# Optimization experiments

Measured on AMD Instinct MI355X. Metric: run time of the kernel, lower is better.

Reference implementation:

```python
import jax, jax.numpy as jnp
import numpy as np

N_NODES = 100000
N_EDGES = 3200000
IN_DIM = 256
HIDDEN = 128
OUT_DIM = 64


def setup_inputs() -> dict:
    key = jax.random.key(0)
    k = jax.random.split(key, 6)
    x = jax.random.normal(k[0], (N_NODES, IN_DIM), dtype=jnp.float32)
    adj_vals = jax.random.uniform(k[1], (N_EDGES,), dtype=jnp.float32)
    # glorot init as in the original
    s1 = np.sqrt(6.0 / (IN_DIM + HIDDEN)).astype(np.float32)
    s2 = np.sqrt(6.0 / (HIDDEN + OUT_DIM)).astype(np.float32)
    w1 = jax.random.uniform(k[2], (IN_DIM, HIDDEN), dtype=jnp.float32, minval=-s1, maxval=s1)
    w2 = jax.random.uniform(k[3], (HIDDEN, OUT_DIM), dtype=jnp.float32, minval=-s2, maxval=s2)
    edge_src = jax.random.randint(k[4], (N_EDGES,), 0, N_NODES, dtype=jnp.int32)
    edge_dst = jax.random.randint(k[5], (N_EDGES,), 0, N_NODES, dtype=jnp.int32)
    return {"x": x, "adj_vals": adj_vals, "w1": w1, "w2": w2,
            "edge_src": edge_src, "edge_dst": edge_dst}


def _spmm(adj_vals, edge_src, edge_dst, h, n_nodes):
    """Sparse adjacency (COO) times dense matrix: out[d] = sum_e vals[e]*h[src[e]]."""
    msgs = adj_vals[:, None] * h[edge_src]  # [E, D] gather + scale
    return jax.ops.segment_sum(msgs, edge_dst, num_segments=n_nodes)


def reference(x, adj_vals, w1, w2, edge_src, edge_dst):
    # Layer 1: pre_sup = X @ W1; support = A @ pre_sup; relu
    h = jax.nn.relu(_spmm(adj_vals, edge_src, edge_dst, x @ w1, N_NODES))
    # Layer 2: identity activation -> logits
    logits = _spmm(adj_vals, edge_src, edge_dst, h @ w2, N_NODES)
    return logits
```

## Files before the change

### kernel.cpp

```cpp
#include <hip/hip_runtime.h>

#define N_NODES 100000
#define N_EDGES 3200000
#define IN_DIM 256
#define HIDDEN 128
#define OUT_DIM 64

#define NBUCK 782
#define CHUNK 3072
#define NPT (CHUNK / 256)
#define NPB ((N_EDGES + CHUNK - 1) / CHUNK)
#define BCAP 6144
#define CURSTRIDE 32

typedef unsigned int uint32;
typedef unsigned short ushort16;

typedef short short8 __attribute__((ext_vector_type(8)));
typedef float f32x4 __attribute__((ext_vector_type(4)));

__device__ __forceinline__ ushort16 f2bf(float f) {
    uint32 u = __float_as_uint(f);
    u += 0x7fffu + ((u >> 16) & 1u);
    return (ushort16)(u >> 16);
}

__device__ __forceinline__ void splitbf(float f, unsigned short& hi, unsigned short& lo) {
    uint32 u = __float_as_uint(f);
    uint32 r = u + 0x7fffu + ((u >> 16) & 1u);
    hi = (unsigned short)(r >> 16);
    float hf = __uint_as_float((r >> 16) << 16);
    float res = f - hf;
    uint32 v = __float_as_uint(res);
    lo = (unsigned short)((v + 0x7fffu + ((v >> 16) & 1u)) >> 16);
}


__global__ __launch_bounds__(256)
void hist_bucket(const int* __restrict__ edst, int* __restrict__ bcnt, int E) {
    __shared__ int h[NBUCK];
    for (int b = threadIdx.x; b < NBUCK; b += 256) h[b] = 0;
    __syncthreads();
    for (int i = blockIdx.x * 256 + threadIdx.x; i < E; i += gridDim.x * 256)
        atomicAdd(&h[edst[i] >> 7], 1);
    __syncthreads();
    for (int b = threadIdx.x; b < NBUCK; b += 256) {
        int c = h[b];
        if (c) atomicAdd(&bcnt[b], c);
    }
}


__global__ __launch_bounds__(256)
void bucket_scan(const int* __restrict__ bcnt, int* __restrict__ bptr,
                 int* __restrict__ cursor, int* __restrict__ row_ptr, int E) {
    __shared__ int st[256];
    int tid = threadIdx.x;
    int v4[4];
    int s0 = 0;
#pragma unroll
    for (int k = 0; k < 4; k++) {
        int b = tid * 4 + k;
        v4[k] = (b < NBUCK) ? bcnt[b] : 0;
        s0 += v4[k];
    }
    st[tid] = s0;
    __syncthreads();
    for (int off = 1; off < 256; off <<= 1) {
        int t = (tid >= off) ? st[tid - off] : 0;
        __syncthreads();
        st[tid] += t;
        __syncthreads();
    }
    int run = st[tid] - s0;
#pragma unroll
    for (int k = 0; k < 4; k++) {
        int b = tid * 4 + k;
        if (b < NBUCK) { bptr[b] = run; cursor[b * CURSTRIDE] = run; }
        run += v4[k];
    }
    if (tid == 255) bptr[NBUCK] = run;
    if (tid == 0) row_ptr[N_NODES] = E;
}


__global__ __launch_bounds__(256)
void bucket_to_csr(const int* __restrict__ bptr, int2* __restrict__ part,
                   int* __restrict__ row_ptr) {
    __shared__ int2 se[BCAP];
    __shared__ int rcnt[128];
    __shared__ int rcur[128];
    int tid = threadIdx.x;
    int b = blockIdx.x;
    int s = bptr[b], e = bptr[b + 1];
    int cnt = min(e - s, BCAP);

    if (tid < 128) rcnt[tid] = 0;
    __syncthreads();
    for (int j = tid; j < cnt; j += 256) {
        int2 p = part[s + j];
        se[j] = p;
        atomicAdd(&rcnt[p.x >> 17], 1);
    }
    __syncthreads();

    int v = (tid < 128) ? rcnt[tid] : 0;
    if (tid < 128) rcur[tid] = v;
    __syncthreads();
    for (int off = 1; off < 128; off <<= 1) {
        int t = 0;
        if (tid < 128 && tid >= off) t = rcur[tid - off];
        __syncthreads();
        if (tid < 128 && tid >= off) rcur[tid] += t;
        __syncthreads();
    }
    if (tid < 128) {
        int excl = rcur[tid] - v;
        rcur[tid] = excl;
        int row = b * 128 + tid;
        if (row < N_NODES) row_ptr[row] = s + excl;
    }
    __syncthreads();

    for (int j = tid; j < cnt; j += 256) {
        int2 p = se[j];
        int r = p.x >> 17;
        int pos = atomicAdd(&rcur[r], 1);
        part[s + pos] = make_int2(p.x & 0x1FFFF, p.y);
    }
}


__global__ __launch_bounds__(256)
void splitw_kernel(const float* __restrict__ w1, const float* __restrict__ w2,
                   unsigned short* __restrict__ w1f_hi, unsigned short* __restrict__ w1f_lo,
                   unsigned short* __restrict__ w2f_hi, unsigned short* __restrict__ w2f_lo) {
    const int W1_SLOTS = (IN_DIM / 32) * (HIDDEN / 16) * 64;
    const int W2_SLOTS = (HIDDEN / 32) * (OUT_DIM / 16) * 64;
    int g = blockIdx.x * 256 + threadIdx.x;
    if (g < W1_SLOTS) {
        int lane = g & 63;
        int rest = g >> 6;
        int nfrag = rest & 7;
        int kblk = rest >> 3;
        int n = nfrag * 16 + (lane & 15);
        int k0 = kblk * 32 + (lane >> 4) * 8;
#pragma unroll
        for (int j = 0; j < 8; j++) {
            unsigned short h, l;
            splitbf(w1[(size_t)(k0 + j) * HIDDEN + n], h, l);
            w1f_hi[(size_t)g * 8 + j] = h;
            w1f_lo[(size_t)g * 8 + j] = l;
        }
    } else if (g < W1_SLOTS + W2_SLOTS) {
        int g2 = g - W1_SLOTS;
        int lane = g2 & 63;
        int rest = g2 >> 6;
        int nfrag = rest & 3;
        int kblk = rest >> 2;
        int n = nfrag * 16 + (lane & 15);
        int k0 = kblk * 32 + (lane >> 4) * 8;
#pragma unroll
        for (int j = 0; j < 8; j++) {
            unsigned short h, l;
            splitbf(w2[(size_t)(k0 + j) * OUT_DIM + n], h, l);
            w2f_hi[(size_t)g2 * 8 + j] = h;
            w2f_lo[(size_t)g2 * 8 + j] = l;
        }
    }
}


template <int K, int BN>
__device__ __forceinline__ void gemm_body(int bx, char* smem, const float* __restrict__ A,
                                          const unsigned short* __restrict__ Bf_hi,
                                          const unsigned short* __restrict__ Bf_lo,
                                          ushort16* __restrict__ C, int M) {
    constexpr int BM = 128, BK = 64;
    constexpr int NF = BN / 32;
    unsigned short* Ah = (unsigned short*)smem;
    unsigned short* Al = (unsigned short*)(smem + BM * BK * 2);

    int tid = threadIdx.x;
    int wid = tid >> 6, lane = tid & 63;
    int wr = wid >> 1, wc = wid & 1;
    int rowBase = bx * BM;
    int r = lane & 15, kg = lane >> 4;
    int swzmask = (lane & 7) << 4;

    f32x4 zero = {0.f, 0.f, 0.f, 0.f};
    f32x4 acc[4][NF];
#pragma unroll
    for (int m = 0; m < 4; m++)
#pragma unroll
        for (int n = 0; n < NF; n++) acc[m][n] = zero;

    int sk4 = (tid & 15) * 4;
    int sm0 = tid >> 4;

    for (int k0 = 0; k0 < K; k0 += BK) {
#pragma unroll
        for (int i = 0; i < 8; i++) {
            int m = sm0 + i * 16;
            int row = rowBase + m;
            float4 f = make_float4(0.f, 0.f, 0.f, 0.f);
            if (row < M) f = *(const float4*)(A + (size_t)row * K + k0 + sk4);
            ushort4 h, l;
            splitbf(f.x, h.x, l.x);
            splitbf(f.y, h.y, l.y);
            splitbf(f.z, h.z, l.z);
            splitbf(f.w, h.w, l.w);
            int bo = (m * BK + sk4) * 2;
            int swz = bo ^ ((m & 7) << 4);
            *(ushort4*)((char*)Ah + swz) = h;
            *(ushort4*)((char*)Al + swz) = l;
        }
        __syncthreads();

#pragma unroll
        for (int kk = 0; kk < BK / 32; kk++) {
            short8 ah[4], al[4];
            int abase = (wr * 64 + r) * (BK * 2) + kk * 64 + kg * 16;
#pragma unroll
            for (int m = 0; m < 4; m++) {
                int swz = (abase + m * (16 * BK * 2)) ^ swzmask;
                ah[m] = *(const short8*)((const char*)Ah + swz);
                al[m] = *(const short8*)((const char*)Al + swz);
            }
            short8 bh[NF], bl[NF];
            int kblk = (k0 >> 5) + kk;
#pragma unroll
            for (int n = 0; n < NF; n++) {
                int nf = wc * NF + n;
                size_t off = ((size_t)(kblk * (BN / 16) + nf) * 64 + lane) * 8;
                bh[n] = *(const short8*)(Bf_hi + off);
                bl[n] = *(const short8*)(Bf_lo + off);
            }
#pragma unroll
            for (int m = 0; m < 4; m++)
#pragma unroll
                for (int n = 0; n < NF; n++) {
                    acc[m][n] = __builtin_amdgcn_mfma_f32_16x16x32_bf16(ah[m], bh[n], acc[m][n], 0, 0, 0);
                    acc[m][n] = __builtin_amdgcn_mfma_f32_16x16x32_bf16(ah[m], bl[n], acc[m][n], 0, 0, 0);
                    acc[m][n] = __builtin_amdgcn_mfma_f32_16x16x32_bf16(al[m], bh[n], acc[m][n], 0, 0, 0);
                }
        }
        __syncthreads();
    }

#pragma unroll
    for (int m = 0; m < 4; m++) {
        int row0 = rowBase + wr * 64 + m * 16 + kg * 4;
#pragma unroll
        for (int j = 0; j < 4; j++) {
            int row = row0 + j;
            if (row < M) {
#pragma unroll
                for (int n = 0; n < NF; n++) {
                    int col = wc * (BN / 2) + n * 16 + r;
                    C[(size_t)row * BN + col] = f2bf(acc[m][n][j]);
                }
            }
        }
    }
}

template <int K, int BN>
__launch_bounds__(256)
__global__ void gemm_mfma(const float* __restrict__ A,
                          const unsigned short* __restrict__ Bf_hi,
                          const unsigned short* __restrict__ Bf_lo,
                          ushort16* __restrict__ C, int M) {
    __shared__ __align__(16) char smem[32768];
    gemm_body<K, BN>(blockIdx.x, smem, A, Bf_hi, Bf_lo, C, M);
}


__launch_bounds__(256)
__global__ void partition_gemm1(const int* __restrict__ esrc, const int* __restrict__ edst,
                                const float* __restrict__ evals, int* __restrict__ cursor,
                                int2* __restrict__ part, int E,
                                const float* __restrict__ A,
                                const unsigned short* __restrict__ w1f_hi,
                                const unsigned short* __restrict__ w1f_lo,
                                ushort16* __restrict__ pre1, int M) {
    __shared__ __align__(16) char smem[40960];
    if (blockIdx.x >= NPB) {
        gemm_body<IN_DIM, HIDDEN>(blockIdx.x - NPB, smem, A, w1f_hi, w1f_lo, pre1, M);
        return;
    }
    int2* sbp  = (int2*)smem;
    unsigned short* sbb = (unsigned short*)(smem + 24576);
    int* hist  = (int*)(smem + 30720);
    int* lst   = (int*)(smem + 33848);
    int* bpos  = (int*)(smem + 36976);

    int tid = threadIdx.x;
    long base = (long)blockIdx.x * CHUNK;
    int cnt = (int)min((long)CHUNK, (long)E - base);

    for (int b = tid; b < NBUCK; b += 256) hist[b] = 0;
    __syncthreads();

    int d[NPT], sv[NPT]; float vv[NPT];
#pragma unroll
    for (int k = 0; k < NPT; k++) {
        int j = tid + k * 256;
        d[k] = -1;
        if (j < cnt) {
            d[k]  = edst[base + j];
            sv[k] = esrc[base + j];
            vv[k] = evals[base + j];
            atomicAdd(&hist[d[k] >> 7], 1);
        }
    }
    __syncthreads();

    if (tid < 64) {
        int c[13];
        int run = 0;
#pragma unroll
        for (int k = 0; k < 13; k++) {
            int b = tid * 13 + k;
            c[k] = (b < NBUCK) ? hist[b] : 0;
            run += c[k];
        }
        int sum = run;
#pragma unroll
        for (int off = 1; off < 64; off <<= 1) {
            int up = __shfl_up(sum, off);
            if (tid >= off) sum += up;
        }
        int excl = sum - run;
#pragma unroll
        for (int k = 0; k < 13; k++) {
            int b = tid * 13 + k;
            if (b < NBUCK) lst[b] = excl;
            excl += c[k];
        }
    }
    __syncthreads();

    for (int b = tid; b < NBUCK; b += 256) {
        int c = hist[b];
        int g = c ? atomicAdd(&cursor[b * CURSTRIDE], c) : 0;
        bpos[b] = g - lst[b];
        hist[b] = lst[b];
    }
    __syncthreads();

#pragma unroll
    for (int k = 0; k < NPT; k++) {
        int j = tid + k * 256;
        if (j < cnt) {
            int dd = d[k], b = dd >> 7;
            int pos = atomicAdd(&hist[b], 1);
            sbb[pos] = (unsigned short)b;
            sbp[pos] = make_int2(sv[k] | ((dd & 127) << 17), __float_as_int(vv[k]));
        }
    }
    __syncthreads();

    for (int j = tid; j < cnt; j += 256)
        part[bpos[sbb[j]] + j] = sbp[j];
}


template <int D, bool RELU>
__launch_bounds__(256)
__global__ void spmm_kernel(const ushort16* __restrict__ feat, const int2* __restrict__ csr_pair,
                            const int* __restrict__ row_ptr, float* __restrict__ out, int n) {
    constexpr int LPR = D * 2 / 16;
    constexpr int EPG = 64 / LPR;
    int wid = threadIdx.x >> 6;
    int lane = threadIdx.x & 63;
    int row = blockIdx.x * 4 + wid;
    if (row >= n) return;
    int s = row_ptr[row], e = row_ptr[row + 1];

    int sub = lane / LPR;
    int slot = lane % LPR;
    const char* fbase = (const char*)feat + slot * 16;

    float acc[8];
#pragma unroll
    for (int j = 0; j < 8; j++) acc[j] = 0.f;

    for (int i = s; i < e; i += 4 * EPG) {
        int2 p[4]; float v[4]; uint4 u[4];
#pragma unroll
        for (int q = 0; q < 4; q++) {
            int ii = i + q * EPG + sub;
            p[q] = csr_pair[min(ii, e - 1)];
            v[q] = (ii < e) ? __int_as_float(p[q].y) : 0.f;
        }
#pragma unroll
        for (int q = 0; q < 4; q++)
            u[q] = *(const uint4*)(fbase + (size_t)p[q].x * (D * 2));
#pragma unroll
        for (int q = 0; q < 4; q++) {
#pragma unroll
            for (int t = 0; t < 4; t++) {
                uint32 w = (&u[q].x)[t];
                acc[2 * t]     += v[q] * __uint_as_float(w << 16);
                acc[2 * t + 1] += v[q] * __uint_as_float(w & 0xffff0000u);
            }
        }
    }

#pragma unroll
    for (int m = LPR; m < 64; m <<= 1) {
#pragma unroll
        for (int j = 0; j < 8; j++) acc[j] += __shfl_xor(acc[j], m);
    }

    if (RELU) {
#pragma unroll
        for (int j = 0; j < 8; j++) acc[j] = acc[j] > 0.f ? acc[j] : 0.f;
    }

    if (lane < LPR) {
        float4* o = (float4*)(out + (size_t)row * D + slot * 8);
        o[0] = make_float4(acc[0], acc[1], acc[2], acc[3]);
        o[1] = make_float4(acc[4], acc[5], acc[6], acc[7]);
    }
}


extern "C" void kernel_launch(void* const* d_in, const int* in_sizes, int n_in,
                              void* d_out, int out_size, void* d_ws, size_t ws_size,
                              hipStream_t stream) {
    const float* x    = (const float*)d_in[0];
    const float* adj  = (const float*)d_in[1];
    const float* w1   = (const float*)d_in[2];
    const float* w2   = (const float*)d_in[3];
    const int*   esrc = (const int*)d_in[4];
    const int*   edst = (const int*)d_in[5];
    float* out = (float*)d_out;

    const int N = N_NODES;
    const int E = N_EDGES;

    char* ws = (char*)d_ws;
    size_t off = 0;
    auto take = [&](size_t bytes) -> char* {
        char* p = ws + off;
        off = (off + bytes + 255) & ~(size_t)255;
        return p;
    };
    int*      bcnt    = (int*)take((size_t)NBUCK * 4);
    int*      bptr    = (int*)take((size_t)(NBUCK + 1) * 4);
    int*      cursor  = (int*)take((size_t)NBUCK * CURSTRIDE * 4);
    int*      row_ptr = (int*)take((size_t)(N + 1) * 4);
    int2*     part    = (int2*)take((size_t)E * 8);
    ushort16* pre1    = (ushort16*)take((size_t)N * HIDDEN * 2);
    ushort16* pre2    = (ushort16*)take((size_t)N * OUT_DIM * 2);
    float*    h       = (float*)take((size_t)N * HIDDEN * 4);
    unsigned short* w1f_hi = (unsigned short*)take((size_t)HIDDEN * IN_DIM * 2);
    unsigned short* w1f_lo = (unsigned short*)take((size_t)HIDDEN * IN_DIM * 2);
    unsigned short* w2f_hi = (unsigned short*)take((size_t)OUT_DIM * HIDDEN * 2);
    unsigned short* w2f_lo = (unsigned short*)take((size_t)OUT_DIM * HIDDEN * 2);

    splitw_kernel<<<20, 256, 0, stream>>>(w1, w2, w1f_hi, w1f_lo, w2f_hi, w2f_lo);

    hipMemsetAsync(bcnt, 0, (size_t)NBUCK * 4, stream);
    hist_bucket<<<1024, 256, 0, stream>>>(edst, bcnt, E);
    bucket_scan<<<1, 256, 0, stream>>>(bcnt, bptr, cursor, row_ptr, E);

    partition_gemm1<<<NPB + (N_NODES + 127) / 128, 256, 0, stream>>>(
        esrc, edst, adj, cursor, part, E, x, w1f_hi, w1f_lo, pre1, N);

    bucket_to_csr<<<NBUCK, 256, 0, stream>>>(bptr, part, row_ptr);

    spmm_kernel<HIDDEN, true><<<(N + 3) / 4, 256, 0, stream>>>(pre1, part, row_ptr, h, N);

    gemm_mfma<HIDDEN, OUT_DIM><<<(N + 127) / 128, 256, 0, stream>>>(h, w2f_hi, w2f_lo, pre2, N);
    spmm_kernel<OUT_DIM, false><<<(N + 3) / 4, 256, 0, stream>>>(pre2, part, row_ptr, out, N);
}
```

Before: 501.7 us.

## Split edge partition into two-level radix pass and deepen SpMM gather pipeline

The single partition pass over 782 destination buckets becomes two passes. The first scatters edges into 13 coarse groups using fewer global cursors and less shared memory. A new pass2 kernel then refines each group into its 64 fine buckets, with the goal of cutting atomic contention and scattered writes. bucket_to_csr now runs with 512 threads, and the SpMM inner loop issues 8 gathers in flight for the 128-wide layer. The cost is an extra full read and write of the edge array, plus higher register pressure in SpMM.

```diff
diff --git a/kernel.cpp b/kernel.cpp
--- a/kernel.cpp
+++ b/kernel.cpp
@@ -12,6 +12,9 @@
 #define NPB ((N_EDGES + CHUNK - 1) / CHUNK)
 #define BCAP 6144
 #define CURSTRIDE 32
+#define NCG 13
+#define CGBITS 13
+#define MAXCH 92
 
 typedef unsigned int uint32;
 typedef unsigned short ushort16;
@@ -53,7 +56,8 @@
 
 __global__ __launch_bounds__(256)
 void bucket_scan(const int* __restrict__ bcnt, int* __restrict__ bptr,
-                 int* __restrict__ cursor, int* __restrict__ row_ptr, int E) {
+                 int* __restrict__ cursor, int* __restrict__ gcur,
+                 int* __restrict__ row_ptr, int E) {
     __shared__ int st[256];
     int tid = threadIdx.x;
     int v4[4];
@@ -73,6 +77,7 @@
         __syncthreads();
     }
     int run = st[tid] - s0;
+    if ((tid & 15) == 0 && (tid >> 4) < NCG) gcur[(tid >> 4) * CURSTRIDE] = run;
 #pragma unroll
     for (int k = 0; k < 4; k++) {
         int b = tid * 4 + k;
@@ -84,7 +89,7 @@
 }
 
 
-__global__ __launch_bounds__(256)
+__global__ __launch_bounds__(512)
 void bucket_to_csr(const int* __restrict__ bptr, int2* __restrict__ part,
                    int* __restrict__ row_ptr) {
     __shared__ int2 se[BCAP];
@@ -97,7 +102,7 @@
 
     if (tid < 128) rcnt[tid] = 0;
     __syncthreads();
-    for (int j = tid; j < cnt; j += 256) {
+    for (int j = tid; j < cnt; j += 512) {
         int2 p = part[s + j];
         se[j] = p;
         atomicAdd(&rcnt[p.x >> 17], 1);
@@ -122,7 +127,7 @@
     }
     __syncthreads();
 
-    for (int j = tid; j < cnt; j += 256) {
+    for (int j = tid; j < cnt; j += 512) {
         int2 p = se[j];
         int r = p.x >> 17;
         int pos = atomicAdd(&rcur[r], 1);
@@ -278,28 +283,28 @@
 
 __launch_bounds__(256)
 __global__ void partition_gemm1(const int* __restrict__ esrc, const int* __restrict__ edst,
-                                const float* __restrict__ evals, int* __restrict__ cursor,
-                                int2* __restrict__ part, int E,
+                                const float* __restrict__ evals, int* __restrict__ gcur,
+                                int2* __restrict__ part2, int E,
                                 const float* __restrict__ A,
                                 const unsigned short* __restrict__ w1f_hi,
                                 const unsigned short* __restrict__ w1f_lo,
                                 ushort16* __restrict__ pre1, int M) {
-    __shared__ __align__(16) char smem[40960];
+    __shared__ __align__(16) char smem[32768];
     if (blockIdx.x >= NPB) {
         gemm_body<IN_DIM, HIDDEN>(blockIdx.x - NPB, smem, A, w1f_hi, w1f_lo, pre1, M);
         return;
     }
-    int2* sbp  = (int2*)smem;
-    unsigned short* sbb = (unsigned short*)(smem + 24576);
-    int* hist  = (int*)(smem + 30720);
-    int* lst   = (int*)(smem + 33848);
-    int* bpos  = (int*)(smem + 36976);
+    int2* sbp = (int2*)smem;
+    unsigned char* sbg = (unsigned char*)(smem + 24576);
+    int* hist = (int*)(smem + 27648);
+    int* lst  = (int*)(smem + 27712);
+    int* bpos = (int*)(smem + 27776);
 
     int tid = threadIdx.x;
     long base = (long)blockIdx.x * CHUNK;
     int cnt = (int)min((long)CHUNK, (long)E - base);
 
-    for (int b = tid; b < NBUCK; b += 256) hist[b] = 0;
+    if (tid < NCG) hist[tid] = 0;
     __syncthreads();
 
     int d[NPT], sv[NPT]; float vv[NPT];
@@ -311,41 +316,93 @@
             d[k]  = edst[base + j];
             sv[k] = esrc[base + j];
             vv[k] = evals[base + j];
-            atomicAdd(&hist[d[k] >> 7], 1);
+            atomicAdd(&hist[d[k] >> CGBITS], 1);
+        }
+    }
+    __syncthreads();
+
+    if (tid == 0) {
+        int run = 0;
+#pragma unroll
+        for (int g = 0; g < NCG; g++) { lst[g] = run; run += hist[g]; }
+    }
+    __syncthreads();
+
+    if (tid < NCG) {
+        int c = hist[tid];
+        int g = c ? atomicAdd(&gcur[tid * CURSTRIDE], c) : 0;
+        bpos[tid] = g - lst[tid];
+        hist[tid] = lst[tid];
+    }
+    __syncthreads();
+
+#pragma unroll
+    for (int k = 0; k < NPT; k++) {
+        int j = tid + k * 256;
+        if (j < cnt) {
+            int dd = d[k], g = dd >> CGBITS;
+            int pos = atomicAdd(&hist[g], 1);
+            sbg[pos] = (unsigned char)g;
+            sbp[pos] = make_int2(sv[k] | ((dd & 8191) << 17), __float_as_int(vv[k]));
+        }
+    }
+    __syncthreads();
+
+    for (int j = tid; j < cnt; j += 256)
+        part2[bpos[sbg[j]] + j] = sbp[j];
+}
+
+
+__global__ __launch_bounds__(256)
+void pass2_kernel(const int2* __restrict__ part2, const int* __restrict__ bptr,
+                  int* __restrict__ cursor, int2* __restrict__ part) {
+    __shared__ __align__(16) int2 sbp[CHUNK];
+    __shared__ unsigned char sbb[CHUNK];
+    __shared__ int hist[64], lst[64], bpos[64];
+    int tid = threadIdx.x;
+    int g = blockIdx.x / MAXCH;
+    int c = blockIdx.x % MAXCH;
+    int gs = bptr[min(64 * g, NBUCK)];
+    int ge = bptr[min(64 * (g + 1), NBUCK)];
+    int base = gs + c * CHUNK;
+    if (base >= ge) return;
+    int cnt = min(CHUNK, ge - base);
+    int b0 = g * 64;
+
+    if (tid < 64) hist[tid] = 0;
+    __syncthreads();
+
+    int lb[NPT]; int2 pp[NPT];
+#pragma unroll
+    for (int k = 0; k < NPT; k++) {
+        int j = tid + k * 256;
+        lb[k] = -1;
+        if (j < cnt) {
+            pp[k] = part2[base + j];
+            int dst = (g << CGBITS) | ((uint32)pp[k].x >> 17);
+            lb[k] = (dst >> 7) - b0;
+            atomicAdd(&hist[lb[k]], 1);
         }
     }
     __syncthreads();
 
     if (tid < 64) {
-        int c[13];
-        int run = 0;
-#pragma unroll
-        for (int k = 0; k < 13; k++) {
-            int b = tid * 13 + k;
-            c[k] = (b < NBUCK) ? hist[b] : 0;
-            run += c[k];
-        }
-        int sum = run;
+        int cc = hist[tid];
+        int sum = cc;
 #pragma unroll
         for (int off = 1; off < 64; off <<= 1) {
             int up = __shfl_up(sum, off);
             if (tid >= off) sum += up;
         }
-        int excl = sum - run;
-#pragma unroll
-        for (int k = 0; k < 13; k++) {
-            int b = tid * 13 + k;
-            if (b < NBUCK) lst[b] = excl;
-            excl += c[k];
-        }
-    }
-    __syncthreads();
-
-    for (int b = tid; b < NBUCK; b += 256) {
-        int c = hist[b];
-        int g = c ? atomicAdd(&cursor[b * CURSTRIDE], c) : 0;
-        bpos[b] = g - lst[b];
-        hist[b] = lst[b];
+        lst[tid] = sum - cc;
+    }
+    __syncthreads();
+
+    if (tid < 64) {
+        int cc = hist[tid];
+        int gp = cc ? atomicAdd(&cursor[(b0 + tid) * CURSTRIDE], cc) : 0;
+        bpos[tid] = gp - lst[tid];
+        hist[tid] = lst[tid];
     }
     __syncthreads();
 
@@ -353,10 +410,11 @@
     for (int k = 0; k < NPT; k++) {
         int j = tid + k * 256;
         if (j < cnt) {
-            int dd = d[k], b = dd >> 7;
+            int b = lb[k];
             int pos = atomicAdd(&hist[b], 1);
-            sbb[pos] = (unsigned short)b;
-            sbp[pos] = make_int2(sv[k] | ((dd & 127) << 17), __float_as_int(vv[k]));
+            sbb[pos] = (unsigned char)b;
+            int dst = (g << CGBITS) | ((uint32)pp[k].x >> 17);
+            sbp[pos] = make_int2((pp[k].x & 0x1FFFF) | ((dst & 127) << 17), pp[k].y);
         }
     }
     __syncthreads();
@@ -372,6 +430,7 @@
                             const int* __restrict__ row_ptr, float* __restrict__ out, int n) {
     constexpr int LPR = D * 2 / 16;
     constexpr int EPG = 64 / LPR;
+    constexpr int DEPTH = (D == 128) ? 8 : 4;
     int wid = threadIdx.x >> 6;
     int lane = threadIdx.x & 63;
     int row = blockIdx.x * 4 + wid;
@@ -386,19 +445,19 @@
 #pragma unroll
     for (int j = 0; j < 8; j++) acc[j] = 0.f;
 
-    for (int i = s; i < e; i += 4 * EPG) {
-        int2 p[4]; float v[4]; uint4 u[4];
-#pragma unroll
-        for (int q = 0; q < 4; q++) {
+    for (int i = s; i < e; i += DEPTH * EPG) {
+        int2 p[DEPTH]; float v[DEPTH]; uint4 u[DEPTH];
+#pragma unroll
+        for (int q = 0; q < DEPTH; q++) {
             int ii = i + q * EPG + sub;
             p[q] = csr_pair[min(ii, e - 1)];
             v[q] = (ii < e) ? __int_as_float(p[q].y) : 0.f;
         }
 #pragma unroll
-        for (int q = 0; q < 4; q++)
+        for (int q = 0; q < DEPTH; q++)
             u[q] = *(const uint4*)(fbase + (size_t)p[q].x * (D * 2));
 #pragma unroll
-        for (int q = 0; q < 4; q++) {
+        for (int q = 0; q < DEPTH; q++) {
 #pragma unroll
             for (int t = 0; t < 4; t++) {
                 uint32 w = (&u[q].x)[t];
@@ -451,8 +510,10 @@
     int*      bcnt    = (int*)take((size_t)NBUCK * 4);
     int*      bptr    = (int*)take((size_t)(NBUCK + 1) * 4);
     int*      cursor  = (int*)take((size_t)NBUCK * CURSTRIDE * 4);
+    int*      gcur    = (int*)take((size_t)NCG * CURSTRIDE * 4);
     int*      row_ptr = (int*)take((size_t)(N + 1) * 4);
     int2*     part    = (int2*)take((size_t)E * 8);
+    int2*     part2   = (int2*)take((size_t)E * 8);
     ushort16* pre1    = (ushort16*)take((size_t)N * HIDDEN * 2);
     ushort16* pre2    = (ushort16*)take((size_t)N * OUT_DIM * 2);
     float*    h       = (float*)take((size_t)N * HIDDEN * 4);
@@ -465,12 +526,14 @@
 
     hipMemsetAsync(bcnt, 0, (size_t)NBUCK * 4, stream);
     hist_bucket<<<1024, 256, 0, stream>>>(edst, bcnt, E);
-    bucket_scan<<<1, 256, 0, stream>>>(bcnt, bptr, cursor, row_ptr, E);
+    bucket_scan<<<1, 256, 0, stream>>>(bcnt, bptr, cursor, gcur, row_ptr, E);
 
     partition_gemm1<<<NPB + (N_NODES + 127) / 128, 256, 0, stream>>>(
-        esrc, edst, adj, cursor, part, E, x, w1f_hi, w1f_lo, pre1, N);
-
-    bucket_to_csr<<<NBUCK, 256, 0, stream>>>(bptr, part, row_ptr);
+        esrc, edst, adj, gcur, part2, E, x, w1f_hi, w1f_lo, pre1, N);
+
+    pass2_kernel<<<NCG * MAXCH, 256, 0, stream>>>(part2, bptr, cursor, part);
+
+    bucket_to_csr<<<NBUCK, 512, 0, stream>>>(bptr, part, row_ptr);
 
     spmm_kernel<HIDDEN, true><<<(N + 3) / 4, 256, 0, stream>>>(pre1, part, row_ptr, h, N);
 
```

Result: faster. 488.1 us (-2.7%).

## Build CSR with per-row global atomics instead of bucketed two-pass partition

Applied to the files above, without the earlier changes.

Replaces the two-level bucket partition (782 buckets of 128 rows plus an in-bucket local sort kernel) with a direct per-row histogram, a three-kernel multi-block prefix scan, and a scatter that uses one global atomicAdd per edge on a per-row cursor. This removes the bucket_to_csr pass and the shared-memory bucketing work inside the fused partition+GEMM kernel. The cost is 3.2M global atomics spread over 100k addresses in both the histogram and the scatter, writes to part that are now random rather than coalesced per bucket, and edge order within a row that is no longer deterministic. It also adds two small kernel launches.

```diff
diff --git a/kernel.cpp b/kernel.cpp
--- a/kernel.cpp
+++ b/kernel.cpp
@@ -6,12 +6,11 @@
 #define HIDDEN 128
 #define OUT_DIM 64
 
-#define NBUCK 782
 #define CHUNK 3072
 #define NPT (CHUNK / 256)
 #define NPB ((N_EDGES + CHUNK - 1) / CHUNK)
-#define BCAP 6144
-#define CURSTRIDE 32
+#define SCB 2048
+#define NSC ((N_NODES + SCB - 1) / SCB)
 
 typedef unsigned int uint32;
 typedef unsigned short ushort16;
@@ -37,34 +36,64 @@
 
 
 __global__ __launch_bounds__(256)
-void hist_bucket(const int* __restrict__ edst, int* __restrict__ bcnt, int E) {
-    __shared__ int h[NBUCK];
-    for (int b = threadIdx.x; b < NBUCK; b += 256) h[b] = 0;
-    __syncthreads();
-    for (int i = blockIdx.x * 256 + threadIdx.x; i < E; i += gridDim.x * 256)
-        atomicAdd(&h[edst[i] >> 7], 1);
-    __syncthreads();
-    for (int b = threadIdx.x; b < NBUCK; b += 256) {
-        int c = h[b];
-        if (c) atomicAdd(&bcnt[b], c);
-    }
+void hist_row(const int* __restrict__ edst, int* __restrict__ rcnt, int E) {
+    int i = blockIdx.x * 256 + threadIdx.x;
+    int stride = gridDim.x * 256;
+    for (; i < E; i += stride)
+        atomicAdd(&rcnt[edst[i]], 1);
 }
 
 
 __global__ __launch_bounds__(256)
-void bucket_scan(const int* __restrict__ bcnt, int* __restrict__ bptr,
-                 int* __restrict__ cursor, int* __restrict__ row_ptr, int E) {
+void scan_rows_a(const int* __restrict__ rcnt, int* __restrict__ bsum) {
     __shared__ int st[256];
     int tid = threadIdx.x;
-    int v4[4];
-    int s0 = 0;
-#pragma unroll
-    for (int k = 0; k < 4; k++) {
-        int b = tid * 4 + k;
-        v4[k] = (b < NBUCK) ? bcnt[b] : 0;
-        s0 += v4[k];
-    }
-    st[tid] = s0;
+    int base = blockIdx.x * SCB + tid * 8;
+    int s = 0;
+#pragma unroll
+    for (int k = 0; k < 8; k++) {
+        int idx = base + k;
+        if (idx < N_NODES) s += rcnt[idx];
+    }
+    st[tid] = s;
+    __syncthreads();
+    for (int off = 128; off > 0; off >>= 1) {
+        if (tid < off) st[tid] += st[tid + off];
+        __syncthreads();
+    }
+    if (tid == 0) bsum[blockIdx.x] = st[0];
+}
+
+__global__ __launch_bounds__(64)
+void scan_rows_b(const int* __restrict__ bsum, int* __restrict__ boff,
+                 int* __restrict__ row_ptr, int E) {
+    int tid = threadIdx.x;
+    int v = (tid < NSC) ? bsum[tid] : 0;
+    int sum = v;
+#pragma unroll
+    for (int off = 1; off < 64; off <<= 1) {
+        int up = __shfl_up(sum, off);
+        if (tid >= off) sum += up;
+    }
+    if (tid < NSC) boff[tid] = sum - v;
+    if (tid == 0) row_ptr[N_NODES] = E;
+}
+
+__global__ __launch_bounds__(256)
+void scan_rows_c(const int* __restrict__ rcnt, const int* __restrict__ boff,
+                 int* __restrict__ row_ptr, int* __restrict__ cursor) {
+    __shared__ int st[256];
+    int tid = threadIdx.x;
+    int base = blockIdx.x * SCB + tid * 8;
+    int v[8];
+    int s = 0;
+#pragma unroll
+    for (int k = 0; k < 8; k++) {
+        int idx = base + k;
+        v[k] = (idx < N_NODES) ? rcnt[idx] : 0;
+        s += v[k];
+    }
+    st[tid] = s;
     __syncthreads();
     for (int off = 1; off < 256; off <<= 1) {
         int t = (tid >= off) ? st[tid - off] : 0;
@@ -72,61 +101,12 @@
         st[tid] += t;
         __syncthreads();
     }
-    int run = st[tid] - s0;
-#pragma unroll
-    for (int k = 0; k < 4; k++) {
-        int b = tid * 4 + k;
-        if (b < NBUCK) { bptr[b] = run; cursor[b * CURSTRIDE] = run; }
-        run += v4[k];
-    }
-    if (tid == 255) bptr[NBUCK] = run;
-    if (tid == 0) row_ptr[N_NODES] = E;
-}
-
-
-__global__ __launch_bounds__(256)
-void bucket_to_csr(const int* __restrict__ bptr, int2* __restrict__ part,
-                   int* __restrict__ row_ptr) {
-    __shared__ int2 se[BCAP];
-    __shared__ int rcnt[128];
-    __shared__ int rcur[128];
-    int tid = threadIdx.x;
-    int b = blockIdx.x;
-    int s = bptr[b], e = bptr[b + 1];
-    int cnt = min(e - s, BCAP);
-
-    if (tid < 128) rcnt[tid] = 0;
-    __syncthreads();
-    for (int j = tid; j < cnt; j += 256) {
-        int2 p = part[s + j];
-        se[j] = p;
-        atomicAdd(&rcnt[p.x >> 17], 1);
-    }
-    __syncthreads();
-
-    int v = (tid < 128) ? rcnt[tid] : 0;
-    if (tid < 128) rcur[tid] = v;
-    __syncthreads();
-    for (int off = 1; off < 128; off <<= 1) {
-        int t = 0;
-        if (tid < 128 && tid >= off) t = rcur[tid - off];
-        __syncthreads();
-        if (tid < 128 && tid >= off) rcur[tid] += t;
-        __syncthreads();
-    }
-    if (tid < 128) {
-        int excl = rcur[tid] - v;
-        rcur[tid] = excl;
-        int row = b * 128 + tid;
-        if (row < N_NODES) row_ptr[row] = s + excl;
-    }
-    __syncthreads();
-
-    for (int j = tid; j < cnt; j += 256) {
-        int2 p = se[j];
-        int r = p.x >> 17;
-        int pos = atomicAdd(&rcur[r], 1);
-        part[s + pos] = make_int2(p.x & 0x1FFFF, p.y);
+    int run = boff[blockIdx.x] + st[tid] - s;
+#pragma unroll
+    for (int k = 0; k < 8; k++) {
+        int idx = base + k;
+        if (idx < N_NODES) { row_ptr[idx] = run; cursor[idx] = run; }
+        run += v[k];
     }
 }
 
@@ -277,30 +257,21 @@
 
 
 __launch_bounds__(256)
-__global__ void partition_gemm1(const int* __restrict__ esrc, const int* __restrict__ edst,
-                                const float* __restrict__ evals, int* __restrict__ cursor,
-                                int2* __restrict__ part, int E,
-                                const float* __restrict__ A,
-                                const unsigned short* __restrict__ w1f_hi,
-                                const unsigned short* __restrict__ w1f_lo,
-                                ushort16* __restrict__ pre1, int M) {
-    __shared__ __align__(16) char smem[40960];
+__global__ void scatter_gemm1(const int* __restrict__ esrc, const int* __restrict__ edst,
+                              const float* __restrict__ evals, int* __restrict__ cursor,
+                              int2* __restrict__ part, int E,
+                              const float* __restrict__ A,
+                              const unsigned short* __restrict__ w1f_hi,
+                              const unsigned short* __restrict__ w1f_lo,
+                              ushort16* __restrict__ pre1, int M) {
+    __shared__ __align__(16) char smem[32768];
     if (blockIdx.x >= NPB) {
         gemm_body<IN_DIM, HIDDEN>(blockIdx.x - NPB, smem, A, w1f_hi, w1f_lo, pre1, M);
         return;
     }
-    int2* sbp  = (int2*)smem;
-    unsigned short* sbb = (unsigned short*)(smem + 24576);
-    int* hist  = (int*)(smem + 30720);
-    int* lst   = (int*)(smem + 33848);
-    int* bpos  = (int*)(smem + 36976);
-
     int tid = threadIdx.x;
     long base = (long)blockIdx.x * CHUNK;
     int cnt = (int)min((long)CHUNK, (long)E - base);
-
-    for (int b = tid; b < NBUCK; b += 256) hist[b] = 0;
-    __syncthreads();
 
     int d[NPT], sv[NPT]; float vv[NPT];
 #pragma unroll
@@ -311,58 +282,15 @@
             d[k]  = edst[base + j];
             sv[k] = esrc[base + j];
             vv[k] = evals[base + j];
-            atomicAdd(&hist[d[k] >> 7], 1);
-        }
-    }
-    __syncthreads();
-
-    if (tid < 64) {
-        int c[13];
-        int run = 0;
-#pragma unroll
-        for (int k = 0; k < 13; k++) {
-            int b = tid * 13 + k;
-            c[k] = (b < NBUCK) ? hist[b] : 0;
-            run += c[k];
-        }
-        int sum = run;
-#pragma unroll
-        for (int off = 1; off < 64; off <<= 1) {
-            int up = __shfl_up(sum, off);
-            if (tid >= off) sum += up;
-        }
-        int excl = sum - run;
-#pragma unroll
-        for (int k = 0; k < 13; k++) {
-            int b = tid * 13 + k;
-            if (b < NBUCK) lst[b] = excl;
-            excl += c[k];
-        }
-    }
-    __syncthreads();
-
-    for (int b = tid; b < NBUCK; b += 256) {
-        int c = hist[b];
-        int g = c ? atomicAdd(&cursor[b * CURSTRIDE], c) : 0;
-        bpos[b] = g - lst[b];
-        hist[b] = lst[b];
-    }
-    __syncthreads();
-
+        }
+    }
 #pragma unroll
     for (int k = 0; k < NPT; k++) {
-        int j = tid + k * 256;
-        if (j < cnt) {
-            int dd = d[k], b = dd >> 7;
-            int pos = atomicAdd(&hist[b], 1);
-            sbb[pos] = (unsigned short)b;
-            sbp[pos] = make_int2(sv[k] | ((dd & 127) << 17), __float_as_int(vv[k]));
-        }
-    }
-    __syncthreads();
-
-    for (int j = tid; j < cnt; j += 256)
-        part[bpos[sbb[j]] + j] = sbp[j];
+        if (d[k] >= 0) {
+            int pos = atomicAdd(&cursor[d[k]], 1);
+            part[pos] = make_int2(sv[k], __float_as_int(vv[k]));
+        }
+    }
 }
 
 
@@ -372,6 +300,7 @@
                             const int* __restrict__ row_ptr, float* __restrict__ out, int n) {
     constexpr int LPR = D * 2 / 16;
     constexpr int EPG = 64 / LPR;
+    constexpr int DEPTH = 4;
     int wid = threadIdx.x >> 6;
     int lane = threadIdx.x & 63;
     int row = blockIdx.x * 4 + wid;
@@ -386,19 +315,19 @@
 #pragma unroll
     for (int j = 0; j < 8; j++) acc[j] = 0.f;
 
-    for (int i = s; i < e; i += 4 * EPG) {
-        int2 p[4]; float v[4]; uint4 u[4];
-#pragma unroll
-        for (int q = 0; q < 4; q++) {
+    for (int i = s; i < e; i += DEPTH * EPG) {
+        int2 p[DEPTH]; float v[DEPTH]; uint4 u[DEPTH];
+#pragma unroll
+        for (int q = 0; q < DEPTH; q++) {
             int ii = i + q * EPG + sub;
             p[q] = csr_pair[min(ii, e - 1)];
             v[q] = (ii < e) ? __int_as_float(p[q].y) : 0.f;
         }
 #pragma unroll
-        for (int q = 0; q < 4; q++)
+        for (int q = 0; q < DEPTH; q++)
             u[q] = *(const uint4*)(fbase + (size_t)p[q].x * (D * 2));
 #pragma unroll
-        for (int q = 0; q < 4; q++) {
+        for (int q = 0; q < DEPTH; q++) {
 #pragma unroll
             for (int t = 0; t < 4; t++) {
                 uint32 w = (&u[q].x)[t];
@@ -448,10 +377,11 @@
         off = (off + bytes + 255) & ~(size_t)255;
         return p;
     };
-    int*      bcnt    = (int*)take((size_t)NBUCK * 4);
-    int*      bptr    = (int*)take((size_t)(NBUCK + 1) * 4);
-    int*      cursor  = (int*)take((size_t)NBUCK * CURSTRIDE * 4);
+    int*      rcnt    = (int*)take((size_t)N * 4);
+    int*      bsum    = (int*)take((size_t)NSC * 4);
+    int*      boff    = (int*)take((size_t)NSC * 4);
     int*      row_ptr = (int*)take((size_t)(N + 1) * 4);
+    int*      cursor  = (int*)take((size_t)N * 4);
     int2*     part    = (int2*)take((size_t)E * 8);
     ushort16* pre1    = (ushort16*)take((size_t)N * HIDDEN * 2);
     ushort16* pre2    = (ushort16*)take((size_t)N * OUT_DIM * 2);
@@ -463,14 +393,14 @@
 
     splitw_kernel<<<20, 256, 0, stream>>>(w1, w2, w1f_hi, w1f_lo, w2f_hi, w2f_lo);
 
-    hipMemsetAsync(bcnt, 0, (size_t)NBUCK * 4, stream);
-    hist_bucket<<<1024, 256, 0, stream>>>(edst, bcnt, E);
-    bucket_scan<<<1, 256, 0, stream>>>(bcnt, bptr, cursor, row_ptr, E);
-
-    partition_gemm1<<<NPB + (N_NODES + 127) / 128, 256, 0, stream>>>(
+    hipMemsetAsync(rcnt, 0, (size_t)N * 4, stream);
+    hist_row<<<2048, 256, 0, stream>>>(edst, rcnt, E);
+    scan_rows_a<<<NSC, 256, 0, stream>>>(rcnt, bsum);
+    scan_rows_b<<<1, 64, 0, stream>>>(bsum, boff, row_ptr, E);
+    scan_rows_c<<<NSC, 256, 0, stream>>>(rcnt, boff, row_ptr, cursor);
+
+    scatter_gemm1<<<NPB + (N_NODES + 127) / 128, 256, 0, stream>>>(
         esrc, edst, adj, cursor, part, E, x, w1f_hi, w1f_lo, pre1, N);
-
-    bucket_to_csr<<<NBUCK, 256, 0, stream>>>(bptr, part, row_ptr);
 
     spmm_kernel<HIDDEN, true><<<(N + 3) / 4, 256, 0, stream>>>(pre1, part, row_ptr, h, N);
 
```

Result: slower. 741.0 us (+47.7%).
